# Kernel optimization log

Measured on AMD Instinct MI355X. Metric: run time of the kernel, lower is better.

Reference implementation:

```python
import jax, jax.numpy as jnp
import numpy as np

HID = 1024   # utter_hidden * 2
UD = 512     # user_dim
B = 16384


def setup_inputs() -> dict:
    key = jax.random.key(0)
    ks = jax.random.split(key, 15)
    sx = 1.0 / np.sqrt(HID)
    sh = 1.0 / np.sqrt(UD)
    inp = {
        'encoder_hidden': jax.random.normal(ks[0], (B, HID), jnp.float32),
        'spk_vectors': jax.random.normal(ks[1], (B, UD), jnp.float32),
        'adr_vectors': jax.random.normal(ks[2], (B, UD), jnp.float32),
    }
    # torch Linear weights are [out, in]; bias=False everywhere
    names_x = ['WA_xr', 'WA_xp', 'WA_xz', 'WA_xh']
    names_h = ['WA_hr', 'WA_hp', 'WA_hz', 'WA_hh']
    names_v = ['VA_hr', 'VA_hp', 'VA_hz', 'VA_hh']
    i = 3
    for n in names_x:
        inp[n] = jax.random.uniform(ks[i], (UD, HID), jnp.float32, -sx, sx); i += 1
    for n in names_h + names_v:
        inp[n] = jax.random.uniform(ks[i], (UD, UD), jnp.float32, -sh, sh); i += 1
    return inp


def reference(encoder_hidden, spk_vectors, adr_vectors,
              WA_xr, WA_xp, WA_xz, WA_xh,
              WA_hr, WA_hp, WA_hz, WA_hh,
              VA_hr, VA_hp, VA_hz, VA_hh):
    def lin(x, W):  # torch nn.Linear (bias=False): x @ W.T
        return x @ W.T
    r_t = jax.nn.sigmoid(lin(encoder_hidden, WA_xr) + lin(spk_vectors, WA_hr) + lin(adr_vectors, VA_hr))
    p_t = jax.nn.sigmoid(lin(encoder_hidden, WA_xp) + lin(spk_vectors, WA_hp) + lin(adr_vectors, VA_hp))
    z_t = jax.nn.sigmoid(lin(encoder_hidden, WA_xz) + lin(spk_vectors, WA_hz) + lin(adr_vectors, VA_hz))
    h_tilde = jnp.tanh(lin(encoder_hidden, WA_xh) + lin(r_t * spk_vectors, WA_hh) + lin(p_t * adr_vectors, VA_hh))
    return (1.0 - z_t) * spk_vectors + z_t * h_tilde
```

## Files before the change

kernel.cpp:

```cpp
#include <hip/hip_runtime.h>
#include <hip/hip_bf16.h>
#include <stdint.h>


typedef short  short8  __attribute__((ext_vector_type(8)));
typedef unsigned short ushort8 __attribute__((ext_vector_type(8)));
typedef float  f32x4   __attribute__((ext_vector_type(4)));

static constexpr int Bn  = 16384;

__device__ __forceinline__ unsigned short f2bf(float x) {
  union { float f; unsigned u; } v; v.f = x;
  unsigned r = v.u + 0x7fffu + ((v.u >> 16) & 1u);
  return (unsigned short)(r >> 16);
}
__device__ __forceinline__ float bf2f(unsigned short h) {
  union { unsigned u; float f; } v; v.u = ((unsigned)h) << 16; return v.f;
}
__device__ __forceinline__ float sigm(float x) { return 1.0f / (1.0f + __expf(-x)); }
__device__ __forceinline__ float tanh_fast(float x) {
  return 2.0f / (1.0f + __expf(-2.0f * x)) - 1.0f;
}

__device__ __forceinline__ void gload_lds16(const void* g, void* l) {
  __builtin_amdgcn_global_load_lds((const __attribute__((address_space(1))) void*)g,
                                   (__attribute__((address_space(3))) void*)l,
                                   16, 0, 0);
}

__global__ __launch_bounds__(256) void pack_all(
    const float* __restrict__ X, const float* __restrict__ S, const float* __restrict__ A,
    const float* __restrict__ xr, const float* __restrict__ xp,
    const float* __restrict__ xz, const float* __restrict__ xh,
    const float* __restrict__ hr, const float* __restrict__ hp, const float* __restrict__ hz,
    const float* __restrict__ vr, const float* __restrict__ vp, const float* __restrict__ vz,
    unsigned short* __restrict__ U, unsigned short* __restrict__ W1)
{
  const int bid = blockIdx.x;
  const int tid = threadIdx.x;
  if (bid < 16384) {
    int idx = bid * 256 + tid;
    int b  = idx >> 8;
    int c8 = (idx & 255) << 3;
    const float* src = (c8 < 1024) ? X + (size_t)b * 1024 + c8
                     : (c8 < 1536) ? S + (size_t)b * 512 + (c8 - 1024)
                                   : A + (size_t)b * 512 + (c8 - 1536);
    f32x4 lo = *(const f32x4*)src;
    f32x4 hi = *(const f32x4*)(src + 4);
    ushort8 o;
    o[0] = f2bf(lo[0]); o[1] = f2bf(lo[1]); o[2] = f2bf(lo[2]); o[3] = f2bf(lo[3]);
    o[4] = f2bf(hi[0]); o[5] = f2bf(hi[1]); o[6] = f2bf(hi[2]); o[7] = f2bf(hi[3]);
    *(ushort8*)&U[(size_t)b * 2048 + c8] = o;
  } else {
    int idx = (bid - 16384) * 256 + tid;
    int n  = idx >> 8;
    int k8 = (idx & 255) << 3;
    int g = n >> 9, j = n & 511;
    const float* src = nullptr;
    if (k8 < 1024) {
      const float* x = (g == 0) ? xr : (g == 1) ? xp : (g == 2) ? xz : xh;
      src = x + (size_t)j * 1024 + k8;
    } else if (k8 < 1536) {
      if (g < 3) { const float* h = (g == 0) ? hr : (g == 1) ? hp : hz; src = h + (size_t)j * 512 + (k8 - 1024); }
    } else {
      if (g < 3) { const float* v = (g == 0) ? vr : (g == 1) ? vp : vz; src = v + (size_t)j * 512 + (k8 - 1536); }
    }
    ushort8 o;
    if (src) { for (int i = 0; i < 8; i++) o[i] = f2bf(src[i]); }
    else     { for (int i = 0; i < 8; i++) o[i] = 0; }
    *(ushort8*)&W1[(size_t)n * 2048 + k8] = o;
  }
}

__global__ __launch_bounds__(256) void pack_w2k(
    const float* __restrict__ hh, const float* __restrict__ vh,
    unsigned short* __restrict__ W2)
{
  int idx = blockIdx.x * 256 + threadIdx.x;
  int n  = idx >> 7;
  int k8 = (idx & 127) << 3;
  const float* src = (k8 < 512) ? hh + (size_t)n * 512 + k8
                                : vh + (size_t)n * 512 + (k8 - 512);
  ushort8 o;
  for (int i = 0; i < 8; i++) o[i] = f2bf(src[i]);
  *(ushort8*)&W2[(size_t)n * 1024 + k8] = o;
}

__global__ __launch_bounds__(512, 1) void gemm256_epi1(
    const unsigned short* __restrict__ Amat,
    const unsigned short* __restrict__ Bmat,
    const int K,
    unsigned short* __restrict__ U2, unsigned short* __restrict__ Zp,
    unsigned short* __restrict__ XHp)
{
  extern __shared__ char lds[];

  const int tid  = threadIdx.x;
  const int lane = tid & 63, wave = tid >> 6;
  const int wm = wave >> 2, wn = wave & 3;
  const int fr = lane & 15, fq = lane >> 4;

  const int k_xcd = blockIdx.x & 7;
  const int i_loc = (int)blockIdx.x >> 3;
  const int n0 = (i_loc & 7) * 256;
  const int m0 = (k_xcd * 8 + (i_loc >> 3)) * 256;

  const int Keff = (n0 >= 1536) ? 1024 : K;
  const int NT   = Keff >> 6;

  const int srow  = tid >> 3;
  const int sslot = (tid & 7) ^ (srow & 7);
  const unsigned short* gA = Amat + (size_t)(m0 + srow) * K + sslot * 8;
  const unsigned short* gB = Bmat + (size_t)(n0 + srow) * K + sslot * 8;
  const size_t K64 = (size_t)64 * K;

  int swz[2];
  swz[0] = ((fq    ) ^ (fr & 7)) << 4;
  swz[1] = ((fq + 4) ^ (fr & 7)) << 4;
  const int aoff = wm * 16384 + fr * 128;
  const int boff = 32768 + wn * 8192 + fr * 128;

  f32x4 acc[8][4] = {};

  auto STAGE = [&](int buf, int tile) {
    const int bufo = buf << 16;
#pragma unroll
    for (int j = 0; j < 4; j++) {
      gload_lds16(gA + (size_t)j * K64 + (tile << 6), lds + bufo + tid * 16 + j * 8192);
      gload_lds16(gB + (size_t)j * K64 + (tile << 6), lds + bufo + 32768 + tid * 16 + j * 8192);
    }
  };
  auto COMPUTE = [&](int buf) {
    const int bufo = buf << 16;
    short8 b[4][2];
#pragma unroll
    for (int ni = 0; ni < 4; ni++)
#pragma unroll
      for (int ks = 0; ks < 2; ks++)
        b[ni][ks] = *(const short8*)(lds + bufo + boff + ni * 2048 + swz[ks]);
#pragma unroll
    for (int c = 0; c < 4; c++) {
      short8 a[2][2];
#pragma unroll
      for (int i = 0; i < 2; i++)
#pragma unroll
        for (int ks = 0; ks < 2; ks++)
          a[i][ks] = *(const short8*)(lds + bufo + aoff + (c * 2 + i) * 2048 + swz[ks]);
#pragma unroll
      for (int i = 0; i < 2; i++)
#pragma unroll
        for (int ni = 0; ni < 4; ni++)
#pragma unroll
          for (int ks = 0; ks < 2; ks++)
            acc[c * 2 + i][ni] = __builtin_amdgcn_mfma_f32_16x16x32_bf16(
                a[i][ks], b[ni][ks], acc[c * 2 + i][ni], 0, 0, 0);
    }
  };

  STAGE(0, 0);
  __syncthreads();

  int cur = 0;
  for (int t = 0; t < NT - 1; ++t) {
    STAGE(cur ^ 1, t + 1);
    COMPUTE(cur);
    __syncthreads();
    cur ^= 1;
  }
  COMPUTE(cur);

#pragma unroll
  for (int mi = 0; mi < 8; mi++) {
#pragma unroll
    for (int ni = 0; ni < 4; ni++) {
      const int ncol = n0 + wn * 64 + ni * 16 + fr;
      const int gate = ncol >> 9, j = ncol & 511;
#pragma unroll
      for (int jj = 0; jj < 4; jj++) {
        const size_t rb = (size_t)(m0 + wm * 128 + mi * 16 + fq * 4 + jj);
        const float v = acc[mi][ni][jj];
        if (gate == 0) {
          const float s = bf2f(Amat[rb * 2048 + 1024 + j]);
          U2[rb * 1024 + j] = f2bf(sigm(v) * s);
        } else if (gate == 1) {
          const float a2 = bf2f(Amat[rb * 2048 + 1536 + j]);
          U2[rb * 1024 + 512 + j] = f2bf(sigm(v) * a2);
        } else if (gate == 2) {
          Zp[rb * 512 + j]  = f2bf(v);
        } else {
          XHp[rb * 512 + j] = f2bf(v);
        }
      }
    }
  }
}

__global__ __launch_bounds__(512, 1) void gemm2_fin(
    const unsigned short* __restrict__ U2,
    const unsigned short* __restrict__ W2,
    const unsigned short* __restrict__ Uu,
    const unsigned short* __restrict__ Zp,
    const unsigned short* __restrict__ XHp, float* __restrict__ Out)
{
  extern __shared__ char lds[];
  constexpr int K = 1024, NT = K >> 6;

  const int tid  = threadIdx.x;
  const int lane = tid & 63, wave = tid >> 6;
  const int wm = wave >> 1, wn = wave & 1;
  const int fr = lane & 15, fq = lane >> 4;

  const int k_xcd = blockIdx.x & 7;
  const int i_loc = (int)blockIdx.x >> 3;
  const int n0 = (i_loc & 3) * 128;
  const int m0 = (k_xcd * 8 + (i_loc >> 2)) * 256;

  const int srow  = tid >> 3;
  const int sslot = (tid & 7) ^ (srow & 7);
  const unsigned short* gA = U2 + (size_t)(m0 + srow) * K + sslot * 8;
  const unsigned short* gB = W2 + (size_t)(n0 + srow) * K + sslot * 8;
  const size_t K64 = (size_t)64 * K;

  int swz[2];
  swz[0] = ((fq    ) ^ (fr & 7)) << 4;
  swz[1] = ((fq + 4) ^ (fr & 7)) << 4;
  const int aoff = wm * 8192 + fr * 128;
  const int boff = 32768 + wn * 8192 + fr * 128;

  f32x4 acc[4][4] = {};

  auto STAGE = [&](int buf, int tile) {
    const int bufo = buf * 49152;
#pragma unroll
    for (int j = 0; j < 4; j++)
      gload_lds16(gA + (size_t)j * K64 + (tile << 6), lds + bufo + tid * 16 + j * 8192);
#pragma unroll
    for (int j = 0; j < 2; j++)
      gload_lds16(gB + (size_t)j * K64 + (tile << 6), lds + bufo + 32768 + tid * 16 + j * 8192);
  };
  auto COMPUTE = [&](int buf) {
    const int bufo = buf * 49152;
    short8 b[4][2];
#pragma unroll
    for (int ni = 0; ni < 4; ni++)
#pragma unroll
      for (int ks = 0; ks < 2; ks++)
        b[ni][ks] = *(const short8*)(lds + bufo + boff + ni * 2048 + swz[ks]);
#pragma unroll
    for (int c = 0; c < 2; c++) {
      short8 a[2][2];
#pragma unroll
      for (int i = 0; i < 2; i++)
#pragma unroll
        for (int ks = 0; ks < 2; ks++)
          a[i][ks] = *(const short8*)(lds + bufo + aoff + (c * 2 + i) * 2048 + swz[ks]);
#pragma unroll
      for (int i = 0; i < 2; i++)
#pragma unroll
        for (int ni = 0; ni < 4; ni++)
#pragma unroll
          for (int ks = 0; ks < 2; ks++)
            acc[c * 2 + i][ni] = __builtin_amdgcn_mfma_f32_16x16x32_bf16(
                a[i][ks], b[ni][ks], acc[c * 2 + i][ni], 0, 0, 0);
    }
  };

  STAGE(0, 0);
  __syncthreads();

  int cur = 0;
  for (int t = 0; t < NT - 1; ++t) {
    STAGE(cur ^ 1, t + 1);
    COMPUTE(cur);
    __syncthreads();
    cur ^= 1;
  }
  COMPUTE(cur);

#pragma unroll
  for (int mt = 0; mt < 4; mt++) {
#pragma unroll
    for (int nt = 0; nt < 4; nt++) {
      const int ncol = n0 + wn * 64 + nt * 16 + fr;
#pragma unroll
      for (int jj = 0; jj < 4; jj++) {
        const size_t rb = (size_t)(m0 + wm * 64 + mt * 16 + fq * 4 + jj);
        const size_t o = rb * 512 + ncol;
        const float z = sigm(bf2f(Zp[o]));
        const float h = tanh_fast(bf2f(XHp[o]) + acc[mt][nt][jj]);
        const float s = bf2f(Uu[rb * 2048 + 1024 + ncol]);
        Out[o] = (1.0f - z) * s + z * h;
      }
    }
  }
}


extern "C" void kernel_launch(void* const* d_in, const int* in_sizes, int n_in,
                              void* d_out, int out_size, void* d_ws, size_t ws_size,
                              hipStream_t stream) {
  const float* X   = (const float*)d_in[0];
  const float* S   = (const float*)d_in[1];
  const float* A   = (const float*)d_in[2];
  const float* Wxr = (const float*)d_in[3];
  const float* Wxp = (const float*)d_in[4];
  const float* Wxz = (const float*)d_in[5];
  const float* Wxh = (const float*)d_in[6];
  const float* Whr = (const float*)d_in[7];
  const float* Whp = (const float*)d_in[8];
  const float* Whz = (const float*)d_in[9];
  const float* Whh = (const float*)d_in[10];
  const float* Vhr = (const float*)d_in[11];
  const float* Vhp = (const float*)d_in[12];
  const float* Vhz = (const float*)d_in[13];
  const float* Vhh = (const float*)d_in[14];

  char* ws = (char*)d_ws;
  size_t off = 0;
  auto alloc = [&](size_t bytes) -> void* {
    void* p = ws + off;
    off += (bytes + 255) & ~(size_t)255;
    return p;
  };
  unsigned short* W1 = (unsigned short*)alloc((size_t)2048 * 2048 * 2);
  unsigned short* W2 = (unsigned short*)alloc((size_t)512 * 1024 * 2);
  unsigned short* U  = (unsigned short*)alloc((size_t)Bn * 2048 * 2);
  unsigned short* U2 = (unsigned short*)alloc((size_t)Bn * 1024 * 2);
  unsigned short* Zp = (unsigned short*)alloc((size_t)Bn * 512 * 2);
  unsigned short* XH = (unsigned short*)alloc((size_t)Bn * 512 * 2);

  pack_all<<<16384 + 2048, 256, 0, stream>>>(
      X, S, A, Wxr, Wxp, Wxz, Wxh, Whr, Whp, Whz, Vhr, Vhp, Vhz, U, W1);
  pack_w2k<<<256, 256, 0, stream>>>(Whh, Vhh, W2);

  (void)hipFuncSetAttribute((const void*)gemm256_epi1,
                            hipFuncAttributeMaxDynamicSharedMemorySize, 131072);
  (void)hipFuncSetAttribute((const void*)gemm2_fin,
                            hipFuncAttributeMaxDynamicSharedMemorySize, 98304);

  gemm256_epi1<<<512, 512, 131072, stream>>>(U, W1, 2048, U2, Zp, XH);

  gemm2_fin<<<256, 512, 98304, stream>>>(U2, W2, U, Zp, XH, (float*)d_out);
}
```

Baseline: 277.5 us.

## Shrink first GEMM to 128x128 tiles with 4 waves and 2 blocks per CU

Changes the first fused GEMM from 256x256 tiles with 8 waves and 128 KB of dynamic LDS to 128x128 tiles with 4 waves and 64 KB of static LDS. It launches 2048 blocks so two can share a CU. The goal is better occupancy and latency hiding, and finer load balance across 256 CUs, since 512 large blocks leave about two waves of work per CU. The cost is less data reuse per tile, which means more global and LDS traffic per FLOP.

```diff
diff --git a/kernel.cpp b/kernel.cpp
--- a/kernel.cpp
+++ b/kernel.cpp
@@ -86,24 +86,24 @@
   *(ushort8*)&W2[(size_t)n * 1024 + k8] = o;
 }
 
-__global__ __launch_bounds__(512, 1) void gemm256_epi1(
+__global__ __launch_bounds__(256, 2) void gemm128_epi1(
     const unsigned short* __restrict__ Amat,
     const unsigned short* __restrict__ Bmat,
     const int K,
     unsigned short* __restrict__ U2, unsigned short* __restrict__ Zp,
     unsigned short* __restrict__ XHp)
 {
-  extern __shared__ char lds[];
+  __shared__ __align__(16) char lds[65536];
 
   const int tid  = threadIdx.x;
   const int lane = tid & 63, wave = tid >> 6;
-  const int wm = wave >> 2, wn = wave & 3;
+  const int wr = wave >> 1, wc = wave & 1;
   const int fr = lane & 15, fq = lane >> 4;
 
   const int k_xcd = blockIdx.x & 7;
   const int i_loc = (int)blockIdx.x >> 3;
-  const int n0 = (i_loc & 7) * 256;
-  const int m0 = (k_xcd * 8 + (i_loc >> 3)) * 256;
+  const int n0 = (i_loc & 15) * 128;
+  const int m0 = (k_xcd * 16 + (i_loc >> 4)) * 128;
 
   const int Keff = (n0 >= 1536) ? 1024 : K;
   const int NT   = Keff >> 6;
@@ -112,49 +112,45 @@
   const int sslot = (tid & 7) ^ (srow & 7);
   const unsigned short* gA = Amat + (size_t)(m0 + srow) * K + sslot * 8;
   const unsigned short* gB = Bmat + (size_t)(n0 + srow) * K + sslot * 8;
-  const size_t K64 = (size_t)64 * K;
+  const size_t K32 = (size_t)32 * K;
 
   int swz[2];
   swz[0] = ((fq    ) ^ (fr & 7)) << 4;
   swz[1] = ((fq + 4) ^ (fr & 7)) << 4;
-  const int aoff = wm * 16384 + fr * 128;
-  const int boff = 32768 + wn * 8192 + fr * 128;
-
-  f32x4 acc[8][4] = {};
+  const int aoff = (wr * 64 + fr) * 128;
+  const int boff = 16384 + (wc * 64 + fr) * 128;
+
+  f32x4 acc[4][4] = {};
 
   auto STAGE = [&](int buf, int tile) {
-    const int bufo = buf << 16;
+    const int bufo = buf << 15;
 #pragma unroll
     for (int j = 0; j < 4; j++) {
-      gload_lds16(gA + (size_t)j * K64 + (tile << 6), lds + bufo + tid * 16 + j * 8192);
-      gload_lds16(gB + (size_t)j * K64 + (tile << 6), lds + bufo + 32768 + tid * 16 + j * 8192);
+      gload_lds16(gA + (size_t)j * K32 + (tile << 6), lds + bufo + j * 4096 + tid * 16);
+      gload_lds16(gB + (size_t)j * K32 + (tile << 6), lds + bufo + 16384 + j * 4096 + tid * 16);
     }
   };
   auto COMPUTE = [&](int buf) {
-    const int bufo = buf << 16;
-    short8 b[4][2];
-#pragma unroll
-    for (int ni = 0; ni < 4; ni++)
+    const int bufo = buf << 15;
+    short8 b[4][2], a[4][2];
+#pragma unroll
+    for (int nt = 0; nt < 4; nt++)
 #pragma unroll
       for (int ks = 0; ks < 2; ks++)
-        b[ni][ks] = *(const short8*)(lds + bufo + boff + ni * 2048 + swz[ks]);
-#pragma unroll
-    for (int c = 0; c < 4; c++) {
-      short8 a[2][2];
-#pragma unroll
-      for (int i = 0; i < 2; i++)
+        b[nt][ks] = *(const short8*)(lds + bufo + boff + nt * 2048 + swz[ks]);
+#pragma unroll
+    for (int mt = 0; mt < 4; mt++)
+#pragma unroll
+      for (int ks = 0; ks < 2; ks++)
+        a[mt][ks] = *(const short8*)(lds + bufo + aoff + mt * 2048 + swz[ks]);
+#pragma unroll
+    for (int mt = 0; mt < 4; mt++)
+#pragma unroll
+      for (int nt = 0; nt < 4; nt++)
 #pragma unroll
         for (int ks = 0; ks < 2; ks++)
-          a[i][ks] = *(const short8*)(lds + bufo + aoff + (c * 2 + i) * 2048 + swz[ks]);
-#pragma unroll
-      for (int i = 0; i < 2; i++)
-#pragma unroll
-        for (int ni = 0; ni < 4; ni++)
-#pragma unroll
-          for (int ks = 0; ks < 2; ks++)
-            acc[c * 2 + i][ni] = __builtin_amdgcn_mfma_f32_16x16x32_bf16(
-                a[i][ks], b[ni][ks], acc[c * 2 + i][ni], 0, 0, 0);
-    }
+          acc[mt][nt] = __builtin_amdgcn_mfma_f32_16x16x32_bf16(
+              a[mt][ks], b[nt][ks], acc[mt][nt], 0, 0, 0);
   };
 
   STAGE(0, 0);
@@ -170,15 +166,15 @@
   COMPUTE(cur);
 
 #pragma unroll
-  for (int mi = 0; mi < 8; mi++) {
-#pragma unroll
-    for (int ni = 0; ni < 4; ni++) {
-      const int ncol = n0 + wn * 64 + ni * 16 + fr;
+  for (int mt = 0; mt < 4; mt++) {
+#pragma unroll
+    for (int nt = 0; nt < 4; nt++) {
+      const int ncol = n0 + wc * 64 + nt * 16 + fr;
       const int gate = ncol >> 9, j = ncol & 511;
 #pragma unroll
       for (int jj = 0; jj < 4; jj++) {
-        const size_t rb = (size_t)(m0 + wm * 128 + mi * 16 + fq * 4 + jj);
-        const float v = acc[mi][ni][jj];
+        const size_t rb = (size_t)(m0 + wr * 64 + mt * 16 + fq * 4 + jj);
+        const float v = acc[mt][nt][jj];
         if (gate == 0) {
           const float s = bf2f(Amat[rb * 2048 + 1024 + j]);
           U2[rb * 1024 + j] = f2bf(sigm(v) * s);
@@ -333,12 +329,10 @@
       X, S, A, Wxr, Wxp, Wxz, Wxh, Whr, Whp, Whz, Vhr, Vhp, Vhz, U, W1);
   pack_w2k<<<256, 256, 0, stream>>>(Whh, Vhh, W2);
 
-  (void)hipFuncSetAttribute((const void*)gemm256_epi1,
-                            hipFuncAttributeMaxDynamicSharedMemorySize, 131072);
   (void)hipFuncSetAttribute((const void*)gemm2_fin,
                             hipFuncAttributeMaxDynamicSharedMemorySize, 98304);
 
-  gemm256_epi1<<<512, 512, 131072, stream>>>(U, W1, 2048, U2, Zp, XH);
+  gemm128_epi1<<<2048, 256, 0, stream>>>(U, W1, 2048, U2, Zp, XH);
 
   gemm2_fin<<<256, 512, 98304, stream>>>(U2, W2, U, Zp, XH, (float*)d_out);
 }
```

Measured after the change: 239.6 us. 13.7% less time.
